# Kernel tuning notes

Hardware: AMD Instinct MI355X
Metric: run time of the kernel (lower is better)

## Reference

```python
import jax, jax.numpy as jnp
import numpy as np
from jax import lax

TAU = 1.0
LAMBDA_CONTRAST = 1.0
GAMMA_ALIGN = 1.0
EPSILON = 0.1
SINKHORN_ITERS = 50
B, V_EN, V_CN, K, H, D = 512, 30000, 20000, 100, 512, 300


def setup_inputs() -> dict:
    key = jax.random.key(0)
    ks = jax.random.split(key, 24)
    s = lambda fan_in: 1.0 / np.sqrt(fan_in)
    inp = {
        'x_bow_en': jax.random.uniform(ks[0], (B, V_EN), jnp.float32),
        'x_bow_cn': jax.random.uniform(ks[1], (B, V_CN), jnp.float32),
        'cluster_ids': jax.random.randint(ks[2], (B,), 0, 9, jnp.int32),
        'eps_en': jax.random.normal(ks[3], (B, K), jnp.float32),
        'eps_cn': jax.random.normal(ks[4], (B, K), jnp.float32),
        # English encoder params
        'W1_en': jax.random.normal(ks[5], (V_EN, H), jnp.float32) * s(V_EN),
        'b1_en': jnp.zeros((H,), jnp.float32),
        'W2_en': jax.random.normal(ks[6], (H, H), jnp.float32) * s(H),
        'b2_en': jnp.zeros((H,), jnp.float32),
        'Wmu_en': jax.random.normal(ks[7], (H, K), jnp.float32) * s(H),
        'bmu_en': jnp.zeros((K,), jnp.float32),
        'Wlv_en': jax.random.normal(ks[8], (H, K), jnp.float32) * s(H),
        'blv_en': jnp.zeros((K,), jnp.float32),
        # Chinese encoder params
        'W1_cn': jax.random.normal(ks[9], (V_CN, H), jnp.float32) * s(V_CN),
        'b1_cn': jnp.zeros((H,), jnp.float32),
        'W2_cn': jax.random.normal(ks[10], (H, H), jnp.float32) * s(H),
        'b2_cn': jnp.zeros((H,), jnp.float32),
        'Wmu_cn': jax.random.normal(ks[11], (H, K), jnp.float32) * s(H),
        'bmu_cn': jnp.zeros((K,), jnp.float32),
        'Wlv_cn': jax.random.normal(ks[12], (H, K), jnp.float32) * s(H),
        'blv_cn': jnp.zeros((K,), jnp.float32),
        # frozen word embeddings + topic embeddings
        'word_emb_en': jax.random.normal(ks[13], (V_EN, D), jnp.float32),
        'word_emb_cn': jax.random.normal(ks[14], (V_CN, D), jnp.float32),
        'topic_emb': jax.random.normal(ks[15], (K, D), jnp.float32),
    }
    return inp


def _encoder(x, eps, W1, b1, W2, b2, Wmu, bmu, Wlv, blv):
    h = jax.nn.softplus(x @ W1 + b1)
    h = jax.nn.softplus(h @ W2 + b2)
    mu = h @ Wmu + bmu
    logvar = h @ Wlv + blv
    z = mu + eps * jnp.exp(0.5 * logvar)  # reparameterization
    theta = jax.nn.softmax(z, axis=-1)
    return theta, mu, logvar


def _compute_beta(word_emb, topic_emb, tau):
    # torch.cdist p=2 -> euclidean distance [V, K]
    sq = (jnp.sum(word_emb ** 2, -1)[:, None] + jnp.sum(topic_emb ** 2, -1)[None, :]
          - 2.0 * word_emb @ topic_emb.T)
    dist = jnp.sqrt(jnp.maximum(sq, 0.0))
    beta = jnp.exp(-dist / tau)
    beta = beta / jnp.sum(beta, axis=0, keepdims=True)  # normalize over vocab
    return beta.T  # [K, V]


def _tm_loss(x_bow, theta, beta, mu, logvar):
    recon = theta @ beta  # [B, V]
    recon_loss = jnp.mean(-jnp.sum(x_bow * jax.nn.log_softmax(recon, axis=-1), axis=-1))
    kl = jnp.mean(0.5 * jnp.sum(jnp.exp(logvar) + mu ** 2 - 1.0 - logvar, axis=-1))
    return recon_loss + kl


def _contrastive_loss(theta_en, theta_cn, cluster_ids, tau):
    b = theta_en.shape[0]
    parity = (jnp.arange(b) % 2 == 0)[:, None]
    thetas = jnp.where(parity, theta_en, theta_cn)  # anchor/other selection
    tn = thetas / jnp.maximum(jnp.linalg.norm(thetas, axis=-1, keepdims=True), 1e-8)
    E = jnp.exp((tn @ tn.T) / tau)  # exp(cos_sim / tau), [B, B]
    offdiag = ~jnp.eye(b, dtype=bool)
    valid = cluster_ids > 0  # falsy cluster -> skipped, matching torch truthiness
    same = cluster_ids[:, None] == cluster_ids[None, :]
    pos_mask = offdiag & same & valid[:, None] & valid[None, :]
    pos_sim = jnp.sum(jnp.where(pos_mask, E, 0.0), axis=1)
    neg_sum = jnp.sum(jnp.where(offdiag, E, 0.0), axis=1)  # all j != i
    has_pos = valid & (jnp.sum(pos_mask, axis=1) > 0)
    per = -jnp.log(pos_sim / (pos_sim + neg_sum + 1e-8))
    loss = jnp.sum(jnp.where(has_pos, per, 0.0))
    count = jnp.sum(has_pos).astype(jnp.float32)
    return loss / (count + 1e-8)


def _sinkhorn(a, b, C, eps):
    Kmat = jnp.exp(-C / eps)
    def step(uv, _):
        u, v = uv
        u = a / (Kmat @ v + 1e-8)
        v = b / (Kmat.T @ u + 1e-8)
        return (u, v), None
    (u, v), _ = lax.scan(step, (jnp.ones_like(a), jnp.ones_like(b)), None, length=SINKHORN_ITERS)
    return u[:, None] * Kmat * v[None, :]


def _alignment_loss(topic_emb, eps):
    tn = topic_emb / jnp.maximum(jnp.linalg.norm(topic_emb, axis=-1, keepdims=True), 1e-8)
    C = 1.0 - tn @ tn.T
    k = topic_emb.shape[0]
    a = jnp.full((k,), 1.0 / k, jnp.float32)
    Q = _sinkhorn(a, a, C, eps)
    return jnp.sum(Q * C)


def reference(x_bow_en, x_bow_cn, cluster_ids, eps_en, eps_cn,
              W1_en, b1_en, W2_en, b2_en, Wmu_en, bmu_en, Wlv_en, blv_en,
              W1_cn, b1_cn, W2_cn, b2_cn, Wmu_cn, bmu_cn, Wlv_cn, blv_cn,
              word_emb_en, word_emb_cn, topic_emb):
    theta_en, mu_en, lv_en = _encoder(x_bow_en, eps_en, W1_en, b1_en, W2_en, b2_en, Wmu_en, bmu_en, Wlv_en, blv_en)
    theta_cn, mu_cn, lv_cn = _encoder(x_bow_cn, eps_cn, W1_cn, b1_cn, W2_cn, b2_cn, Wmu_cn, bmu_cn, Wlv_cn, blv_cn)
    beta_en = _compute_beta(word_emb_en, topic_emb, TAU)
    beta_cn = _compute_beta(word_emb_cn, topic_emb, TAU)
    tm_en = _tm_loss(x_bow_en, theta_en, beta_en, mu_en, lv_en)
    tm_cn = _tm_loss(x_bow_cn, theta_cn, beta_cn, mu_cn, lv_cn)
    contrast = _contrastive_loss(theta_en, theta_cn, cluster_ids, TAU)
    align = _alignment_loss(topic_emb, EPSILON)
    total = tm_en + tm_cn + LAMBDA_CONTRAST * contrast + GAMMA_ALIGN * align
    return total, tm_en, tm_cn, contrast, align, theta_en, theta_cn, beta_en, beta_cn
```

## Files before the change

### kernel.cpp

```cpp
#include <hip/hip_runtime.h>
#include <math.h>

#define BATCH 512
#define VEN 30000
#define VCN 20000
#define KT 100
#define HID 512
#define DIM 300
#define VENP 30080
#define VCNP 20096
#define KDP 320
#define VENK 30080
#define VCNK 20096

typedef float f32x4 __attribute__((ext_vector_type(4)));
typedef short bf16x8 __attribute__((ext_vector_type(8)));
typedef unsigned short u16x8 __attribute__((ext_vector_type(8)));
typedef unsigned int u32;

#define WS_H1_EN   0
#define WS_H2_EN   (WS_H1_EN + 262144)
#define WS_H1_CN   (WS_H2_EN + 262144)
#define WS_H2_CN   (WS_H1_CN + 262144)
#define WS_ROWS_EN (WS_H2_CN + 262144)
#define WS_ROWS_CN (WS_ROWS_EN + 1536)
#define WS_SCAL    (WS_ROWS_CN + 1536)
#define ZERO_FLOATS (WS_SCAL + 64)
#define WS_BIG     ZERO_FLOATS
#define XB_EN      WS_BIG
#define XB_CN      (WS_BIG + 7700480)
#define WEP_EN     WS_BIG
#define WEP_CN     (WS_BIG + 4812800)
#define TEP        (WS_BIG + 4812800 + 3215360)
#define BT_EN      (WS_BIG + 8048640)
#define BT_CN      (BT_EN + 1925120)
#define THP_EN     (BT_CN + 1286144)
#define THP_CN     (THP_EN + 32768)
#define AFTER_BIG  (WS_BIG + 12845056)
#define W1T_EN     AFTER_BIG
#define W1T_CN     (W1T_EN + 7700480)
#define W2T_EN     (W1T_CN + 5144576)
#define W2T_CN     (W2T_EN + 131072)
#define H1B_EN     (W2T_CN + 131072)
#define H1B_CN     (H1B_EN + 131072)
#define WN2_EN     (H1B_CN + 131072)
#define WN2_CN     (WN2_EN + 30080)
#define TN2        (WN2_CN + 20096)
#define WS_TNBUF   (TN2 + 128)
#define WS_TNT     (WS_TNBUF + 51200)
#define WS_CTOP    (WS_TNT + 30000)
#define WS_COLSUM_EN (WS_CTOP + 10000)
#define WS_COLSUM_CN (WS_COLSUM_EN + 128)

#define OUT_THETA_EN 5
#define OUT_THETA_CN (OUT_THETA_EN + 51200)
#define OUT_BETA_EN  (OUT_THETA_CN + 51200)
#define OUT_BETA_CN  (OUT_BETA_EN + 3000000)

__device__ __forceinline__ float waveReduceSum(float v) {
    #pragma unroll
    for (int o = 32; o > 0; o >>= 1) v += __shfl_down(v, o);
    return v;
}

__device__ __forceinline__ unsigned short f2bf(float f) {
    unsigned int u = __float_as_uint(f);
    u = (u + 0x7FFFu + ((u >> 16) & 1u)) >> 16;
    return (unsigned short)u;
}

__device__ __forceinline__ void gl2lds16(const unsigned short* g, unsigned short* l) {
    __builtin_amdgcn_global_load_lds(
        (const __attribute__((address_space(1))) u32*)g,
        (__attribute__((address_space(3))) u32*)l, 16, 0, 0);
}

__global__ __launch_bounds__(256)
void cast_pad_bf16_kernel(const float* __restrict__ src, unsigned short* __restrict__ dst,
                          int cols, int colsPad)
{
    int row = blockIdx.y;
    int col = (blockIdx.x * 256 + threadIdx.x) * 8;
    if (col >= colsPad) return;
    u16x8 o = {0,0,0,0,0,0,0,0};
    if (col < cols) {
        float4 a = *(const float4*)&src[(size_t)row * cols + col];
        float4 b = *(const float4*)&src[(size_t)row * cols + col + 4];
        o = (u16x8){ f2bf(a.x), f2bf(a.y), f2bf(a.z), f2bf(a.w),
                     f2bf(b.x), f2bf(b.y), f2bf(b.z), f2bf(b.w) };
    }
    *(u16x8*)&dst[(size_t)row * colsPad + col] = o;
}

template <int MODE>
__global__ __launch_bounds__(256)
void gemm_async(const unsigned short* __restrict__ A, const unsigned short* __restrict__ B,
                float* __restrict__ C, int N, int ldA, int ldB, int chunkK, int K,
                int Mreal, const float* __restrict__ an2, const float* __restrict__ bn2)
{
    __shared__ __align__(16) unsigned short As[128 * 64];
    __shared__ __align__(16) unsigned short Bs[128 * 64];
    const int tid = threadIdx.x;
    const int m0 = blockIdx.x * 128, n0 = blockIdx.y * 128;
    const int kStart = blockIdx.z * chunkK;
    const int kEnd = min(kStart + chunkK, K);

    const int wave = tid >> 6, lane = tid & 63;
    const int wm = (wave & 1) * 64, wn = (wave >> 1) * 64;
    const int l15 = lane & 15, quad = lane >> 4;

    const int rl = lane >> 3;
    const int cs = (lane & 7) ^ rl;

    f32x4 acc[4][4];
    #pragma unroll
    for (int i = 0; i < 4; ++i)
        #pragma unroll
        for (int j = 0; j < 4; ++j)
            acc[i][j] = (f32x4){0.f, 0.f, 0.f, 0.f};

    for (int k0 = kStart; k0 < kEnd; k0 += 64) {
        #pragma unroll
        for (int j = 0; j < 4; ++j) {
            int seg = wave * 4 + j;
            int r = seg * 8 + rl;
            gl2lds16(A + (size_t)(m0 + r) * ldA + k0 + cs * 8, &As[seg * 512]);
            gl2lds16(B + (size_t)(n0 + r) * ldB + k0 + cs * 8, &Bs[seg * 512]);
        }
        asm volatile("s_waitcnt vmcnt(0)" ::: "memory");
        __syncthreads();

        #pragma unroll
        for (int kh = 0; kh < 2; ++kh) {
            bf16x8 af[4], bfr[4];
            #pragma unroll
            for (int mi = 0; mi < 4; ++mi) {
                int r = wm + mi * 16 + l15;
                af[mi] = *(const bf16x8*)&As[r * 64 + (((kh << 2) | quad) ^ (r & 7)) * 8];
            }
            #pragma unroll
            for (int ni = 0; ni < 4; ++ni) {
                int r = wn + ni * 16 + l15;
                bfr[ni] = *(const bf16x8*)&Bs[r * 64 + (((kh << 2) | quad) ^ (r & 7)) * 8];
            }
            #pragma unroll
            for (int mi = 0; mi < 4; ++mi)
                #pragma unroll
                for (int ni = 0; ni < 4; ++ni)
                    acc[mi][ni] = __builtin_amdgcn_mfma_f32_16x16x32_bf16(af[mi], bfr[ni], acc[mi][ni], 0, 0, 0);
        }
        __syncthreads();
    }

    #pragma unroll
    for (int mi = 0; mi < 4; ++mi)
        #pragma unroll
        for (int ni = 0; ni < 4; ++ni)
            #pragma unroll
            for (int i = 0; i < 4; ++i) {
                int m = m0 + wm + mi * 16 + quad * 4 + i;
                int n = n0 + wn + ni * 16 + l15;
                if (MODE == 0) {
                    atomicAdd(&C[(size_t)m * N + n], acc[mi][ni][i]);
                } else if (MODE == 1) {
                    C[(size_t)m * N + n] = acc[mi][ni][i];
                } else {
                    if (m < Mreal && n < KT) {
                        float sq = an2[m] + bn2[n] - 2.f * acc[mi][ni][i];
                        C[(size_t)n * Mreal + m] = __expf(-sqrtf(fmaxf(sq, 0.f)));
                    }
                }
            }
}

__global__ __launch_bounds__(256)
void recon_mfma_kernel(const unsigned short* __restrict__ A, const unsigned short* __restrict__ B,
                       const float* __restrict__ x, int V, float* __restrict__ rows)
{
    __shared__ __align__(16) unsigned short As[128 * 64];
    __shared__ __align__(16) unsigned short Bs[128 * 64];
    const int tid = threadIdx.x;
    const int m0 = blockIdx.x * 128, n0 = blockIdx.y * 128;
    const int wave = tid >> 6, lane = tid & 63;
    const int wm = (wave & 1) * 64, wn = (wave >> 1) * 64;
    const int l15 = lane & 15, quad = lane >> 4;
    const int rl = lane >> 3;
    const int cs = (lane & 7) ^ rl;

    f32x4 acc[4][4];
    #pragma unroll
    for (int i = 0; i < 4; ++i)
        #pragma unroll
        for (int j = 0; j < 4; ++j)
            acc[i][j] = (f32x4){0.f, 0.f, 0.f, 0.f};

    for (int k0 = 0; k0 < 128; k0 += 64) {
        #pragma unroll
        for (int j = 0; j < 4; ++j) {
            int seg = wave * 4 + j;
            int r = seg * 8 + rl;
            gl2lds16(A + (size_t)(m0 + r) * 128 + k0 + cs * 8, &As[seg * 512]);
            gl2lds16(B + (size_t)(n0 + r) * 128 + k0 + cs * 8, &Bs[seg * 512]);
        }
        asm volatile("s_waitcnt vmcnt(0)" ::: "memory");
        __syncthreads();

        #pragma unroll
        for (int kh = 0; kh < 2; ++kh) {
            bf16x8 af[4], bfr[4];
            #pragma unroll
            for (int mi = 0; mi < 4; ++mi) {
                int r = wm + mi * 16 + l15;
                af[mi] = *(const bf16x8*)&As[r * 64 + (((kh << 2) | quad) ^ (r & 7)) * 8];
            }
            #pragma unroll
            for (int ni = 0; ni < 4; ++ni) {
                int r = wn + ni * 16 + l15;
                bfr[ni] = *(const bf16x8*)&Bs[r * 64 + (((kh << 2) | quad) ^ (r & 7)) * 8];
            }
            #pragma unroll
            for (int mi = 0; mi < 4; ++mi)
                #pragma unroll
                for (int ni = 0; ni < 4; ++ni)
                    acc[mi][ni] = __builtin_amdgcn_mfma_f32_16x16x32_bf16(af[mi], bfr[ni], acc[mi][ni], 0, 0, 0);
        }
        __syncthreads();
    }

    #pragma unroll
    for (int ni = 0; ni < 4; ++ni) {
        int b = n0 + wn + ni * 16 + l15;
        float tse = 0.f, tsxr = 0.f, tsx = 0.f;
        #pragma unroll
        for (int mi = 0; mi < 4; ++mi) {
            int v0 = m0 + wm + mi * 16 + quad * 4;
            if (v0 + 3 < V) {
                float4 xv = *(const float4*)&x[(size_t)b * V + v0];
                float xa[4] = {xv.x, xv.y, xv.z, xv.w};
                #pragma unroll
                for (int i = 0; i < 4; ++i) {
                    float r = acc[mi][ni][i];
                    tse += __expf(r);
                    tsxr += xa[i] * r;
                    tsx  += xa[i];
                }
            } else {
                #pragma unroll
                for (int i = 0; i < 4; ++i) {
                    int v = v0 + i;
                    if (v < V) {
                        float xv1 = x[(size_t)b * V + v];
                        float r = acc[mi][ni][i];
                        tse += __expf(r); tsxr += xv1 * r; tsx += xv1;
                    }
                }
            }
        }
        tse  += __shfl_xor(tse, 16);  tse  += __shfl_xor(tse, 32);
        tsxr += __shfl_xor(tsxr, 16); tsxr += __shfl_xor(tsxr, 32);
        tsx  += __shfl_xor(tsx, 16);  tsx  += __shfl_xor(tsx, 32);
        if (quad == 0) {
            atomicAdd(&rows[b], tse);
            atomicAdd(&rows[512 + b], tsxr);
            atomicAdd(&rows[1024 + b], tsx);
        }
    }
}

__global__ __launch_bounds__(256)
void transpose_cast_kernel(const float* __restrict__ src, unsigned short* __restrict__ dst,
                           int K, int N, int Kp)
{
    __shared__ float tile[32][33];
    int kb = blockIdx.x * 32, nb = blockIdx.y * 32;
    int tx = threadIdx.x & 31, ty4 = threadIdx.x >> 5;
    #pragma unroll
    for (int j = 0; j < 4; ++j) {
        int k = kb + ty4 * 4 + j;
        tile[ty4 * 4 + j][tx] = (k < K) ? src[(size_t)k * N + nb + tx] : 0.f;
    }
    __syncthreads();
    #pragma unroll
    for (int j = 0; j < 4; ++j) {
        int n = nb + ty4 * 4 + j;
        int k = kb + tx;
        if (k < Kp) dst[(size_t)n * Kp + k] = f2bf(tile[tx][ty4 * 4 + j]);
    }
}

__global__ void padcast_sqnorm_kernel(const float* __restrict__ src, unsigned short* __restrict__ dst,
                                      float* __restrict__ n2, int V)
{
    int m = blockIdx.x, tid = threadIdx.x;
    float sq = 0.f;
    #pragma unroll
    for (int j = 0; j < 5; ++j) {
        int k = tid + j * 64;
        float v = (m < V && k < DIM) ? src[(size_t)m * DIM + k] : 0.f;
        dst[(size_t)m * KDP + k] = f2bf(v);
        sq += v * v;
    }
    sq = waveReduceSum(sq);
    if (tid == 0) n2[m] = sq;
}

__global__ __launch_bounds__(256)
void normbeta_bt_kernel(float* __restrict__ beta, const float* __restrict__ cs,
                        unsigned short* __restrict__ bt, int V)
{
    int v = blockIdx.x * 64 + (threadIdx.x & 63);
    int kq = threadIdx.x >> 6;
    unsigned short tmp[32];
    #pragma unroll
    for (int j = 0; j < 32; ++j) {
        int k = kq * 32 + j;
        float val = 0.f;
        if (k < KT && v < V) {
            val = beta[(size_t)k * V + v] * (1.0f / cs[k]);
            beta[(size_t)k * V + v] = val;
        }
        tmp[j] = f2bf(val);
    }
    #pragma unroll
    for (int q = 0; q < 4; ++q)
        *(u16x8*)&bt[(size_t)v * 128 + kq * 32 + q * 8] = *(u16x8*)&tmp[q * 8];
}

__global__ void theta_pad_kernel(const float* __restrict__ theta, unsigned short* __restrict__ thp)
{
    int idx = blockIdx.x * 256 + threadIdx.x;
    int b = idx >> 7, k = idx & 127;
    thp[idx] = f2bf(k < KT ? theta[b * KT + k] : 0.f);
}

__global__ __launch_bounds__(256)
void colsum_kernel(const float* __restrict__ bta, float* __restrict__ cs, int V)
{
    int k = blockIdx.x, tid = threadIdx.x;
    float s = 0.f;
    for (int v = tid; v < V; v += 256) s += bta[(size_t)k * V + v];
    s = waveReduceSum(s);
    __shared__ float cw[4];
    if ((tid & 63) == 0) cw[tid >> 6] = s;
    __syncthreads();
    if (tid == 0) cs[k] = cw[0] + cw[1] + cw[2] + cw[3];
}

__global__ void bias_softplus_bf16_kernel(const float* __restrict__ src, const float* __restrict__ b,
                                          unsigned short* __restrict__ dst, int n)
{
    int i = blockIdx.x * 256 + threadIdx.x;
    if (i < n) {
        float x = src[i] + b[i & (HID - 1)];
        float sp = fmaxf(x, 0.f) + log1pf(__expf(-fabsf(x)));
        dst[i] = f2bf(sp);
    }
}

__global__ void bias_softplus_f32_kernel(float* __restrict__ y, const float* __restrict__ b, int n)
{
    int i = blockIdx.x * 256 + threadIdx.x;
    if (i < n) {
        float x = y[i] + b[i & (HID - 1)];
        y[i] = fmaxf(x, 0.f) + log1pf(__expf(-fabsf(x)));
    }
}

__global__ __launch_bounds__(128)
void encoder_head_kernel(const float* __restrict__ h2, const float* __restrict__ Wmu,
                         const float* __restrict__ bmu, const float* __restrict__ Wlv,
                         const float* __restrict__ blv, const float* __restrict__ eps,
                         float* __restrict__ theta_out, float* __restrict__ kl_accum)
{
    int i = blockIdx.x, tid = threadIdx.x;
    __shared__ float hrow[HID];
    __shared__ float sred[128];
    #pragma unroll
    for (int j = 0; j < 4; ++j) hrow[tid + 128 * j] = h2[i * HID + tid + 128 * j];
    __syncthreads();
    float mu = 0.f, lv = 0.f;
    if (tid < KT) {
        #pragma unroll 8
        for (int h = 0; h < HID; ++h) {
            float hv = hrow[h];
            mu += hv * Wmu[h * KT + tid];
            lv += hv * Wlv[h * KT + tid];
        }
        mu += bmu[tid]; lv += blv[tid];
    }
    float z = (tid < KT) ? (mu + eps[i * KT + tid] * __expf(0.5f * lv)) : -3.0e38f;
    sred[tid] = z; __syncthreads();
    for (int s = 64; s > 0; s >>= 1) { if (tid < s) sred[tid] = fmaxf(sred[tid], sred[tid + s]); __syncthreads(); }
    float zmax = sred[0]; __syncthreads();
    float e = (tid < KT) ? __expf(z - zmax) : 0.f;
    sred[tid] = e; __syncthreads();
    for (int s = 64; s > 0; s >>= 1) { if (tid < s) sred[tid] += sred[tid + s]; __syncthreads(); }
    float esum = sred[0]; __syncthreads();
    if (tid < KT) theta_out[i * KT + tid] = e / esum;
    float kterm = (tid < KT) ? 0.5f * (__expf(lv) + mu * mu - 1.f - lv) : 0.f;
    sred[tid] = kterm; __syncthreads();
    for (int s = 64; s > 0; s >>= 1) { if (tid < s) sred[tid] += sred[tid + s]; __syncthreads(); }
    if (tid == 0) atomicAdd(kl_accum, sred[0]);
}

__global__ __launch_bounds__(256)
void recon_finalize_kernel(const float* __restrict__ rows_en, const float* __restrict__ rows_cn,
                           float* __restrict__ scal)
{
    const float* rows = (blockIdx.x == 0) ? rows_en : rows_cn;
    int tid = threadIdx.x;
    float s = 0.f;
    for (int r = tid; r < 512; r += 256) {
        float se = rows[r], sxr = rows[512 + r], sx = rows[1024 + r];
        s += __logf(se) * sx - sxr;
    }
    s = waveReduceSum(s);
    __shared__ float cw[4];
    if ((tid & 63) == 0) cw[tid >> 6] = s;
    __syncthreads();
    if (tid == 0) scal[5 + blockIdx.x] = cw[0] + cw[1] + cw[2] + cw[3];
}

__global__ __launch_bounds__(128)
void contrast_prep_kernel(const float* __restrict__ theta_en, const float* __restrict__ theta_cn,
                          float* __restrict__ tn)
{
    int i = blockIdx.x, tid = threadIdx.x;
    const float* src = ((i & 1) == 0) ? theta_en : theta_cn;
    float val = (tid < KT) ? src[i * KT + tid] : 0.f;
    __shared__ float sred[128];
    sred[tid] = val * val; __syncthreads();
    for (int s = 64; s > 0; s >>= 1) { if (tid < s) sred[tid] += sred[tid + s]; __syncthreads(); }
    float inv = 1.0f / fmaxf(sqrtf(sred[0]), 1e-8f);
    if (tid < KT) tn[i * KT + tid] = val * inv;
}

__global__ __launch_bounds__(256)
void contrast_main_kernel(const float* __restrict__ tn, const int* __restrict__ cid,
                          float* __restrict__ scal)
{
    int i = blockIdx.x, tid = threadIdx.x;
    __shared__ __align__(16) float ti[KT];
    if (tid < KT) ti[tid] = tn[i * KT + tid];
    __syncthreads();
    int ci = cid[i];
    bool vi = ci > 0;
    float pos = 0.f, neg = 0.f, pcnt = 0.f;
    for (int j = tid; j < 512; j += 256) {
        if (j == i) continue;
        float s = 0.f;
        const float4* tj = reinterpret_cast<const float4*>(&tn[j * KT]);
        #pragma unroll
        for (int q = 0; q < 25; ++q) {
            float4 t4 = tj[q];
            s += ti[4 * q] * t4.x + ti[4 * q + 1] * t4.y + ti[4 * q + 2] * t4.z + ti[4 * q + 3] * t4.w;
        }
        float E = __expf(s);
        neg += E;
        if (vi && cid[j] == ci) { pos += E; pcnt += 1.f; }
    }
    pos = waveReduceSum(pos); neg = waveReduceSum(neg); pcnt = waveReduceSum(pcnt);
    __shared__ float cw[3][4];
    int w = tid >> 6;
    if ((tid & 63) == 0) { cw[0][w] = pos; cw[1][w] = neg; cw[2][w] = pcnt; }
    __syncthreads();
    if (tid == 0) {
        float P = 0.f, N = 0.f, PC = 0.f;
        for (int q = 0; q < 4; ++q) { P += cw[0][q]; N += cw[1][q]; PC += cw[2][q]; }
        if (vi && PC > 0.f) {
            atomicAdd(&scal[2], -__logf(P / (P + N + 1e-8f)));
            atomicAdd(&scal[3], 1.0f);
        }
    }
}

__global__ void norm_rows_kernel(const float* __restrict__ A, float* __restrict__ out, int cols)
{
    int r = blockIdx.x, tid = threadIdx.x;
    float s = 0.f;
    for (int d = tid; d < cols; d += 64) { float a = A[r * cols + d]; s += a * a; }
    s = waveReduceSum(s);
    s = __shfl(s, 0);
    float inv = 1.0f / fmaxf(sqrtf(s), 1e-8f);
    for (int d = tid; d < cols; d += 64) out[r * cols + d] = A[r * cols + d] * inv;
}

__global__ __launch_bounds__(128)
void ctopic_kernel(const float* __restrict__ tnt, float* __restrict__ C)
{
    int i = blockIdx.x, tid = threadIdx.x;
    __shared__ float ti[DIM];
    for (int d = tid; d < DIM; d += 128) ti[d] = tnt[i * DIM + d];
    __syncthreads();
    for (int j = tid; j < KT; j += 128) {
        float s = 0.f;
        for (int d = 0; d < DIM; ++d) s += ti[d] * tnt[j * DIM + d];
        C[i * KT + j] = 1.0f - s;
    }
}

__global__ __launch_bounds__(256, 1)
void sinkhorn_kernel(const float* __restrict__ C, float* __restrict__ scal)
{
    __shared__ __align__(16) float ub[128], vb[128];
    __shared__ float cw[4];
    const int tid = threadIdx.x;
    const bool gA = (tid < 100);
    const bool gB = (tid >= 128 && tid < 228);
    const int rc = gA ? tid : (tid - 128);

    float kk[100];
    if (gA) {
        #pragma unroll
        for (int j = 0; j < 100; ++j) kk[j] = __expf(-10.f * C[rc * 100 + j]);
    } else if (gB) {
        #pragma unroll
        for (int j = 0; j < 100; ++j) kk[j] = __expf(-10.f * C[j * 100 + rc]);
    }
    if (tid < 128) { ub[tid] = 1.f; vb[tid] = 1.f; }
    __syncthreads();

    for (int it = 0; it < 50; ++it) {
        if (gA) {
            float s = 0.f;
            #pragma unroll
            for (int q = 0; q < 25; ++q) {
                float4 v4 = *(const float4*)&vb[q * 4];
                s += kk[q*4]*v4.x + kk[q*4+1]*v4.y + kk[q*4+2]*v4.z + kk[q*4+3]*v4.w;
            }
            ub[rc] = 0.01f / (s + 1e-8f);
        }
        __syncthreads();
        if (gB) {
            float s = 0.f;
            #pragma unroll
            for (int q = 0; q < 25; ++q) {
                float4 u4 = *(const float4*)&ub[q * 4];
                s += kk[q*4]*u4.x + kk[q*4+1]*u4.y + kk[q*4+2]*u4.z + kk[q*4+3]*u4.w;
            }
            vb[rc] = 0.01f / (s + 1e-8f);
        }
        __syncthreads();
    }

    float part = 0.f;
    if (gA) {
        float u = ub[rc];
        #pragma unroll
        for (int j = 0; j < 100; ++j) {
            float k = kk[j];
            part += u * k * vb[j] * (-0.1f * __logf(k));
        }
    }
    part = waveReduceSum(part);
    if ((tid & 63) == 0) cw[tid >> 6] = part;
    __syncthreads();
    if (tid == 0) scal[4] = cw[0] + cw[1] + cw[2] + cw[3];
}

__global__ void final_combine_kernel(const float* __restrict__ scal, float* __restrict__ out)
{
    if (threadIdx.x == 0 && blockIdx.x == 0) {
        const float invB = 1.0f / 512.0f;
        float tm_en = scal[5] * invB + scal[0] * invB;
        float tm_cn = scal[6] * invB + scal[1] * invB;
        float contrast = scal[2] / (scal[3] + 1e-8f);
        float align = scal[4];
        out[0] = tm_en + tm_cn + contrast + align;
        out[1] = tm_en;
        out[2] = tm_cn;
        out[3] = contrast;
        out[4] = align;
    }
}

extern "C" void kernel_launch(void* const* d_in, const int* in_sizes, int n_in,
                              void* d_out_v, int out_size, void* d_ws, size_t ws_size,
                              hipStream_t stream)
{
    const float* x_en   = (const float*)d_in[0];
    const float* x_cn   = (const float*)d_in[1];
    const int*   cid    = (const int*)  d_in[2];
    const float* eps_en = (const float*)d_in[3];
    const float* eps_cn = (const float*)d_in[4];
    const float* W1_en  = (const float*)d_in[5];
    const float* b1_en  = (const float*)d_in[6];
    const float* W2_en  = (const float*)d_in[7];
    const float* b2_en  = (const float*)d_in[8];
    const float* Wmu_en = (const float*)d_in[9];
    const float* bmu_en = (const float*)d_in[10];
    const float* Wlv_en = (const float*)d_in[11];
    const float* blv_en = (const float*)d_in[12];
    const float* W1_cn  = (const float*)d_in[13];
    const float* b1_cn  = (const float*)d_in[14];
    const float* W2_cn  = (const float*)d_in[15];
    const float* b2_cn  = (const float*)d_in[16];
    const float* Wmu_cn = (const float*)d_in[17];
    const float* bmu_cn = (const float*)d_in[18];
    const float* Wlv_cn = (const float*)d_in[19];
    const float* blv_cn = (const float*)d_in[20];
    const float* we_en  = (const float*)d_in[21];
    const float* we_cn  = (const float*)d_in[22];
    const float* te     = (const float*)d_in[23];
    float* out = (float*)d_out_v;
    float* ws  = (float*)d_ws;

    unsigned short* w1t_en = (unsigned short*)(ws + W1T_EN);
    unsigned short* w1t_cn = (unsigned short*)(ws + W1T_CN);
    unsigned short* w2t_en = (unsigned short*)(ws + W2T_EN);
    unsigned short* w2t_cn = (unsigned short*)(ws + W2T_CN);
    unsigned short* h1b_en = (unsigned short*)(ws + H1B_EN);
    unsigned short* h1b_cn = (unsigned short*)(ws + H1B_CN);
    unsigned short* xb_en  = (unsigned short*)(ws + XB_EN);
    unsigned short* xb_cn  = (unsigned short*)(ws + XB_CN);
    unsigned short* wep_en = (unsigned short*)(ws + WEP_EN);
    unsigned short* wep_cn = (unsigned short*)(ws + WEP_CN);
    unsigned short* tep    = (unsigned short*)(ws + TEP);
    unsigned short* bt_en  = (unsigned short*)(ws + BT_EN);
    unsigned short* bt_cn  = (unsigned short*)(ws + BT_CN);
    unsigned short* thp_en = (unsigned short*)(ws + THP_EN);
    unsigned short* thp_cn = (unsigned short*)(ws + THP_CN);

    hipMemsetAsync(d_ws, 0, (size_t)ZERO_FLOATS * sizeof(float), stream);

    cast_pad_bf16_kernel<<<dim3(15, 512), 256, 0, stream>>>(x_en, xb_en, VEN, VENK);
    cast_pad_bf16_kernel<<<dim3(10, 512), 256, 0, stream>>>(x_cn, xb_cn, VCN, VCNK);

    transpose_cast_kernel<<<dim3(940, 16), 256, 0, stream>>>(W1_en, w1t_en, VEN, HID, VENK);
    transpose_cast_kernel<<<dim3(628, 16), 256, 0, stream>>>(W1_cn, w1t_cn, VCN, HID, VCNK);
    transpose_cast_kernel<<<dim3(16, 16), 256, 0, stream>>>(W2_en, w2t_en, HID, HID, HID);
    transpose_cast_kernel<<<dim3(16, 16), 256, 0, stream>>>(W2_cn, w2t_cn, HID, HID, HID);

    gemm_async<0><<<dim3(4, 4, 47), 256, 0, stream>>>(xb_en, w1t_en, ws + WS_H1_EN,
        HID, VENK, VENK, 640, VENK, 0, nullptr, nullptr);
    gemm_async<0><<<dim3(4, 4, 32), 256, 0, stream>>>(xb_cn, w1t_cn, ws + WS_H1_CN,
        HID, VCNK, VCNK, 640, VCNK, 0, nullptr, nullptr);

    bias_softplus_bf16_kernel<<<1024, 256, 0, stream>>>(ws + WS_H1_EN, b1_en, h1b_en, 262144);
    bias_softplus_bf16_kernel<<<1024, 256, 0, stream>>>(ws + WS_H1_CN, b1_cn, h1b_cn, 262144);

    gemm_async<1><<<dim3(4, 4, 1), 256, 0, stream>>>(h1b_en, w2t_en, ws + WS_H2_EN,
        HID, HID, HID, HID, HID, 0, nullptr, nullptr);
    gemm_async<1><<<dim3(4, 4, 1), 256, 0, stream>>>(h1b_cn, w2t_cn, ws + WS_H2_CN,
        HID, HID, HID, HID, HID, 0, nullptr, nullptr);

    bias_softplus_f32_kernel<<<1024, 256, 0, stream>>>(ws + WS_H2_EN, b2_en, 262144);
    bias_softplus_f32_kernel<<<1024, 256, 0, stream>>>(ws + WS_H2_CN, b2_cn, 262144);

    encoder_head_kernel<<<BATCH, 128, 0, stream>>>(ws + WS_H2_EN, Wmu_en, bmu_en, Wlv_en, blv_en,
                                                   eps_en, out + OUT_THETA_EN, ws + WS_SCAL + 0);
    encoder_head_kernel<<<BATCH, 128, 0, stream>>>(ws + WS_H2_CN, Wmu_cn, bmu_cn, Wlv_cn, blv_cn,
                                                   eps_cn, out + OUT_THETA_CN, ws + WS_SCAL + 1);

    padcast_sqnorm_kernel<<<VENP, 64, 0, stream>>>(we_en, wep_en, ws + WN2_EN, VEN);
    padcast_sqnorm_kernel<<<VCNP, 64, 0, stream>>>(we_cn, wep_cn, ws + WN2_CN, VCN);
    padcast_sqnorm_kernel<<<128, 64, 0, stream>>>(te, tep, ws + TN2, KT);

    gemm_async<2><<<dim3(235, 1, 1), 256, 0, stream>>>(wep_en, tep, out + OUT_BETA_EN,
        128, KDP, KDP, KDP, KDP, VEN, ws + WN2_EN, ws + TN2);
    gemm_async<2><<<dim3(157, 1, 1), 256, 0, stream>>>(wep_cn, tep, out + OUT_BETA_CN,
        128, KDP, KDP, KDP, KDP, VCN, ws + WN2_CN, ws + TN2);

    colsum_kernel<<<KT, 256, 0, stream>>>(out + OUT_BETA_EN, ws + WS_COLSUM_EN, VEN);
    colsum_kernel<<<KT, 256, 0, stream>>>(out + OUT_BETA_CN, ws + WS_COLSUM_CN, VCN);

    normbeta_bt_kernel<<<VENP / 64, 256, 0, stream>>>(out + OUT_BETA_EN, ws + WS_COLSUM_EN, bt_en, VEN);
    normbeta_bt_kernel<<<VCNP / 64, 256, 0, stream>>>(out + OUT_BETA_CN, ws + WS_COLSUM_CN, bt_cn, VCN);

    theta_pad_kernel<<<256, 256, 0, stream>>>(out + OUT_THETA_EN, thp_en);
    theta_pad_kernel<<<256, 256, 0, stream>>>(out + OUT_THETA_CN, thp_cn);

    recon_mfma_kernel<<<dim3(VENP / 128, 4), 256, 0, stream>>>(bt_en, thp_en, x_en, VEN, ws + WS_ROWS_EN);
    recon_mfma_kernel<<<dim3(VCNP / 128, 4), 256, 0, stream>>>(bt_cn, thp_cn, x_cn, VCN, ws + WS_ROWS_CN);
    recon_finalize_kernel<<<2, 256, 0, stream>>>(ws + WS_ROWS_EN, ws + WS_ROWS_CN, ws + WS_SCAL);

    contrast_prep_kernel<<<BATCH, 128, 0, stream>>>(out + OUT_THETA_EN, out + OUT_THETA_CN, ws + WS_TNBUF);
    contrast_main_kernel<<<BATCH, 256, 0, stream>>>(ws + WS_TNBUF, cid, ws + WS_SCAL);

    norm_rows_kernel<<<KT, 64, 0, stream>>>(te, ws + WS_TNT, DIM);
    ctopic_kernel<<<KT, 128, 0, stream>>>(ws + WS_TNT, ws + WS_CTOP);
    sinkhorn_kernel<<<1, 256, 0, stream>>>(ws + WS_CTOP, ws + WS_SCAL);

    final_combine_kernel<<<1, 64, 0, stream>>>(ws + WS_SCAL, out);
}
```

Baseline: 887.7 us.

## Merge independent kernels into wide dependency-level launches via block-index dispatch

Replaces about thirty separate kernel launches with roughly nine, each dispatching on block index to the work of one dependency level. Unrelated jobs such as the en/cn encoder stages, beta GEMMs, sinkhorn and the contrastive loss now run concurrently in one grid. Small per-row kernels are repacked so each 256-thread block covers four rows. The aim is to cut launch overhead and fill the GPU during small serial phases. The cost is heterogeneous blocks: every block carries the largest branch's LDS allocation, which can lower occupancy, and a long single-block task such as sinkhorn can set the tail of its launch.

```diff
diff --git a/kernel.cpp b/kernel.cpp
--- a/kernel.cpp
+++ b/kernel.cpp
@@ -75,12 +75,13 @@
         (__attribute__((address_space(3))) u32*)l, 16, 0, 0);
 }
 
-__global__ __launch_bounds__(256)
-void cast_pad_bf16_kernel(const float* __restrict__ src, unsigned short* __restrict__ dst,
-                          int cols, int colsPad)
-{
-    int row = blockIdx.y;
-    int col = (blockIdx.x * 256 + threadIdx.x) * 8;
+
+__device__ __forceinline__ void cast_pad_core(const float* __restrict__ src,
+                                              unsigned short* __restrict__ dst,
+                                              int cols, int colsPad, int nx, int vb)
+{
+    int row = vb / nx, cb = vb - row * nx;
+    int col = (cb * 256 + (int)threadIdx.x) * 8;
     if (col >= colsPad) return;
     u16x8 o = {0,0,0,0,0,0,0,0};
     if (col < cols) {
@@ -92,23 +93,37 @@
     *(u16x8*)&dst[(size_t)row * colsPad + col] = o;
 }
 
+__device__ __forceinline__ void transpose_core(const float* __restrict__ src,
+                                               unsigned short* __restrict__ dst,
+                                               int K, int N, int Kp, int kb, int nb,
+                                               float (*tile)[33])
+{
+    int tx = threadIdx.x & 31, ty4 = threadIdx.x >> 5;
+    #pragma unroll
+    for (int j = 0; j < 4; ++j) {
+        int k = kb + ty4 * 4 + j;
+        tile[ty4 * 4 + j][tx] = (k < K) ? src[(size_t)k * N + nb + tx] : 0.f;
+    }
+    __syncthreads();
+    #pragma unroll
+    for (int j = 0; j < 4; ++j) {
+        int n = nb + ty4 * 4 + j;
+        int k = kb + tx;
+        if (k < Kp) dst[(size_t)n * Kp + k] = f2bf(tile[tx][ty4 * 4 + j]);
+    }
+}
+
 template <int MODE>
-__global__ __launch_bounds__(256)
-void gemm_async(const unsigned short* __restrict__ A, const unsigned short* __restrict__ B,
-                float* __restrict__ C, int N, int ldA, int ldB, int chunkK, int K,
-                int Mreal, const float* __restrict__ an2, const float* __restrict__ bn2)
-{
-    __shared__ __align__(16) unsigned short As[128 * 64];
-    __shared__ __align__(16) unsigned short Bs[128 * 64];
+__device__ __forceinline__ void gemm_core(
+    const unsigned short* __restrict__ A, const unsigned short* __restrict__ B,
+    float* __restrict__ C, int N, int ldA, int ldB, int kStart, int kEnd,
+    int Mreal, const float* __restrict__ an2, const float* __restrict__ bn2,
+    int m0, int n0, unsigned short* As, unsigned short* Bs)
+{
     const int tid = threadIdx.x;
-    const int m0 = blockIdx.x * 128, n0 = blockIdx.y * 128;
-    const int kStart = blockIdx.z * chunkK;
-    const int kEnd = min(kStart + chunkK, K);
-
     const int wave = tid >> 6, lane = tid & 63;
     const int wm = (wave & 1) * 64, wn = (wave >> 1) * 64;
     const int l15 = lane & 15, quad = lane >> 4;
-
     const int rl = lane >> 3;
     const int cs = (lane & 7) ^ rl;
 
@@ -173,14 +188,12 @@
             }
 }
 
-__global__ __launch_bounds__(256)
-void recon_mfma_kernel(const unsigned short* __restrict__ A, const unsigned short* __restrict__ B,
-                       const float* __restrict__ x, int V, float* __restrict__ rows)
-{
-    __shared__ __align__(16) unsigned short As[128 * 64];
-    __shared__ __align__(16) unsigned short Bs[128 * 64];
+__device__ __forceinline__ void recon_core(
+    const unsigned short* __restrict__ A, const unsigned short* __restrict__ B,
+    const float* __restrict__ x, int V, float* __restrict__ rows,
+    int m0, int n0, unsigned short* As, unsigned short* Bs)
+{
     const int tid = threadIdx.x;
-    const int m0 = blockIdx.x * 128, n0 = blockIdx.y * 128;
     const int wave = tid >> 6, lane = tid & 63;
     const int wm = (wave & 1) * 64, wn = (wave >> 1) * 64;
     const int l15 = lane & 15, quad = lane >> 4;
@@ -267,48 +280,112 @@
     }
 }
 
-__global__ __launch_bounds__(256)
-void transpose_cast_kernel(const float* __restrict__ src, unsigned short* __restrict__ dst,
-                           int K, int N, int Kp)
-{
-    __shared__ float tile[32][33];
-    int kb = blockIdx.x * 32, nb = blockIdx.y * 32;
-    int tx = threadIdx.x & 31, ty4 = threadIdx.x >> 5;
-    #pragma unroll
-    for (int j = 0; j < 4; ++j) {
-        int k = kb + ty4 * 4 + j;
-        tile[ty4 * 4 + j][tx] = (k < K) ? src[(size_t)k * N + nb + tx] : 0.f;
-    }
-    __syncthreads();
-    #pragma unroll
-    for (int j = 0; j < 4; ++j) {
-        int n = nb + ty4 * 4 + j;
-        int k = kb + tx;
-        if (k < Kp) dst[(size_t)n * Kp + k] = f2bf(tile[tx][ty4 * 4 + j]);
-    }
-}
-
-__global__ void padcast_sqnorm_kernel(const float* __restrict__ src, unsigned short* __restrict__ dst,
-                                      float* __restrict__ n2, int V)
-{
-    int m = blockIdx.x, tid = threadIdx.x;
+__device__ __forceinline__ void padcast4_core(const float* __restrict__ src,
+                                              unsigned short* __restrict__ dst,
+                                              float* __restrict__ n2, int V, int vb)
+{
+    int w = threadIdx.x >> 6, lane = threadIdx.x & 63;
+    int m = vb * 4 + w;
     float sq = 0.f;
     #pragma unroll
     for (int j = 0; j < 5; ++j) {
-        int k = tid + j * 64;
+        int k = lane + j * 64;
         float v = (m < V && k < DIM) ? src[(size_t)m * DIM + k] : 0.f;
         dst[(size_t)m * KDP + k] = f2bf(v);
         sq += v * v;
     }
     sq = waveReduceSum(sq);
-    if (tid == 0) n2[m] = sq;
-}
-
-__global__ __launch_bounds__(256)
-void normbeta_bt_kernel(float* __restrict__ beta, const float* __restrict__ cs,
-                        unsigned short* __restrict__ bt, int V)
-{
-    int v = blockIdx.x * 64 + (threadIdx.x & 63);
+    if (lane == 0) n2[m] = sq;
+}
+
+__device__ __forceinline__ void norm_rows4_core(const float* __restrict__ A,
+                                                float* __restrict__ out, int vb)
+{
+    int w = threadIdx.x >> 6, lane = threadIdx.x & 63;
+    int r = vb * 4 + w;
+    float s = 0.f;
+    for (int d = lane; d < DIM; d += 64) { float a = A[r * DIM + d]; s += a * a; }
+    s = waveReduceSum(s);
+    s = __shfl(s, 0);
+    float inv = 1.0f / fmaxf(sqrtf(s), 1e-8f);
+    for (int d = lane; d < DIM; d += 64) out[r * DIM + d] = A[r * DIM + d] * inv;
+}
+
+__device__ __forceinline__ void bias_sp_bf16_core(const float* __restrict__ src,
+                                                  const float* __restrict__ b,
+                                                  unsigned short* __restrict__ dst, int vb)
+{
+    int i = vb * 256 + threadIdx.x;
+    float x = src[i] + b[i & (HID - 1)];
+    float sp = fmaxf(x, 0.f) + log1pf(__expf(-fabsf(x)));
+    dst[i] = f2bf(sp);
+}
+
+__device__ __forceinline__ void bias_sp_f32_core(float* __restrict__ y,
+                                                 const float* __restrict__ b, int vb)
+{
+    int i = vb * 256 + threadIdx.x;
+    float x = y[i] + b[i & (HID - 1)];
+    y[i] = fmaxf(x, 0.f) + log1pf(__expf(-fabsf(x)));
+}
+
+__device__ __forceinline__ void encoder_head_core(
+    const float* __restrict__ h2, const float* __restrict__ Wmu, const float* __restrict__ bmu,
+    const float* __restrict__ Wlv, const float* __restrict__ blv, const float* __restrict__ eps,
+    float* __restrict__ theta_out, float* __restrict__ kl_accum, int i,
+    float* hrow, float* red, float* lvb)
+{
+    int tid = threadIdx.x;
+    hrow[tid] = h2[i * HID + tid];
+    hrow[tid + 256] = h2[i * HID + tid + 256];
+    __syncthreads();
+    bool gA = tid < KT;
+    bool gB = (tid >= 128) && (tid < 128 + KT);
+    int rc = gA ? tid : (tid - 128);
+    float acc = 0.f;
+    if (gA || gB) {
+        const float* W = gA ? Wmu : Wlv;
+        #pragma unroll 8
+        for (int h = 0; h < HID; ++h) acc += hrow[h] * W[h * KT + rc];
+        acc += gA ? bmu[rc] : blv[rc];
+    }
+    if (gB) lvb[rc] = acc;
+    __syncthreads();
+    float z = -3.0e38f, kterm = 0.f;
+    if (gA) {
+        float lv = lvb[rc], mu = acc;
+        z = mu + eps[i * KT + rc] * __expf(0.5f * lv);
+        kterm = 0.5f * (__expf(lv) + mu * mu - 1.f - lv);
+    }
+    red[tid] = z; __syncthreads();
+    for (int s = 128; s > 0; s >>= 1) { if (tid < s) red[tid] = fmaxf(red[tid], red[tid + s]); __syncthreads(); }
+    float zmax = red[0]; __syncthreads();
+    float e = gA ? __expf(z - zmax) : 0.f;
+    red[tid] = e; __syncthreads();
+    for (int s = 128; s > 0; s >>= 1) { if (tid < s) red[tid] += red[tid + s]; __syncthreads(); }
+    float esum = red[0]; __syncthreads();
+    if (gA) theta_out[i * KT + rc] = e / esum;
+    red[tid] = gA ? kterm : 0.f; __syncthreads();
+    for (int s = 128; s > 0; s >>= 1) { if (tid < s) red[tid] += red[tid + s]; __syncthreads(); }
+    if (tid == 0) atomicAdd(kl_accum, red[0]);
+}
+
+__device__ __forceinline__ void colsum_core(const float* __restrict__ bta,
+                                            float* __restrict__ cs, int V, int k, float* cw)
+{
+    int tid = threadIdx.x;
+    float s = 0.f;
+    for (int v = tid; v < V; v += 256) s += bta[(size_t)k * V + v];
+    s = waveReduceSum(s);
+    if ((tid & 63) == 0) cw[tid >> 6] = s;
+    __syncthreads();
+    if (tid == 0) cs[k] = cw[0] + cw[1] + cw[2] + cw[3];
+}
+
+__device__ __forceinline__ void normbeta_core(float* __restrict__ beta, const float* __restrict__ cs,
+                                              unsigned short* __restrict__ bt, int V, int vb)
+{
+    int v = vb * 64 + (threadIdx.x & 63);
     int kq = threadIdx.x >> 6;
     unsigned short tmp[32];
     #pragma unroll
@@ -326,121 +403,37 @@
         *(u16x8*)&bt[(size_t)v * 128 + kq * 32 + q * 8] = *(u16x8*)&tmp[q * 8];
 }
 
-__global__ void theta_pad_kernel(const float* __restrict__ theta, unsigned short* __restrict__ thp)
-{
-    int idx = blockIdx.x * 256 + threadIdx.x;
+__device__ __forceinline__ void theta_pad_core(const float* __restrict__ theta,
+                                               unsigned short* __restrict__ thp, int vb)
+{
+    int idx = vb * 256 + threadIdx.x;
     int b = idx >> 7, k = idx & 127;
     thp[idx] = f2bf(k < KT ? theta[b * KT + k] : 0.f);
 }
 
-__global__ __launch_bounds__(256)
-void colsum_kernel(const float* __restrict__ bta, float* __restrict__ cs, int V)
-{
-    int k = blockIdx.x, tid = threadIdx.x;
-    float s = 0.f;
-    for (int v = tid; v < V; v += 256) s += bta[(size_t)k * V + v];
-    s = waveReduceSum(s);
-    __shared__ float cw[4];
-    if ((tid & 63) == 0) cw[tid >> 6] = s;
-    __syncthreads();
-    if (tid == 0) cs[k] = cw[0] + cw[1] + cw[2] + cw[3];
-}
-
-__global__ void bias_softplus_bf16_kernel(const float* __restrict__ src, const float* __restrict__ b,
-                                          unsigned short* __restrict__ dst, int n)
-{
-    int i = blockIdx.x * 256 + threadIdx.x;
-    if (i < n) {
-        float x = src[i] + b[i & (HID - 1)];
-        float sp = fmaxf(x, 0.f) + log1pf(__expf(-fabsf(x)));
-        dst[i] = f2bf(sp);
-    }
-}
-
-__global__ void bias_softplus_f32_kernel(float* __restrict__ y, const float* __restrict__ b, int n)
-{
-    int i = blockIdx.x * 256 + threadIdx.x;
-    if (i < n) {
-        float x = y[i] + b[i & (HID - 1)];
-        y[i] = fmaxf(x, 0.f) + log1pf(__expf(-fabsf(x)));
-    }
-}
-
-__global__ __launch_bounds__(128)
-void encoder_head_kernel(const float* __restrict__ h2, const float* __restrict__ Wmu,
-                         const float* __restrict__ bmu, const float* __restrict__ Wlv,
-                         const float* __restrict__ blv, const float* __restrict__ eps,
-                         float* __restrict__ theta_out, float* __restrict__ kl_accum)
-{
-    int i = blockIdx.x, tid = threadIdx.x;
-    __shared__ float hrow[HID];
-    __shared__ float sred[128];
-    #pragma unroll
-    for (int j = 0; j < 4; ++j) hrow[tid + 128 * j] = h2[i * HID + tid + 128 * j];
-    __syncthreads();
-    float mu = 0.f, lv = 0.f;
-    if (tid < KT) {
-        #pragma unroll 8
-        for (int h = 0; h < HID; ++h) {
-            float hv = hrow[h];
-            mu += hv * Wmu[h * KT + tid];
-            lv += hv * Wlv[h * KT + tid];
-        }
-        mu += bmu[tid]; lv += blv[tid];
-    }
-    float z = (tid < KT) ? (mu + eps[i * KT + tid] * __expf(0.5f * lv)) : -3.0e38f;
-    sred[tid] = z; __syncthreads();
-    for (int s = 64; s > 0; s >>= 1) { if (tid < s) sred[tid] = fmaxf(sred[tid], sred[tid + s]); __syncthreads(); }
-    float zmax = sred[0]; __syncthreads();
-    float e = (tid < KT) ? __expf(z - zmax) : 0.f;
-    sred[tid] = e; __syncthreads();
-    for (int s = 64; s > 0; s >>= 1) { if (tid < s) sred[tid] += sred[tid + s]; __syncthreads(); }
-    float esum = sred[0]; __syncthreads();
-    if (tid < KT) theta_out[i * KT + tid] = e / esum;
-    float kterm = (tid < KT) ? 0.5f * (__expf(lv) + mu * mu - 1.f - lv) : 0.f;
-    sred[tid] = kterm; __syncthreads();
-    for (int s = 64; s > 0; s >>= 1) { if (tid < s) sred[tid] += sred[tid + s]; __syncthreads(); }
-    if (tid == 0) atomicAdd(kl_accum, sred[0]);
-}
-
-__global__ __launch_bounds__(256)
-void recon_finalize_kernel(const float* __restrict__ rows_en, const float* __restrict__ rows_cn,
-                           float* __restrict__ scal)
-{
-    const float* rows = (blockIdx.x == 0) ? rows_en : rows_cn;
+__device__ __forceinline__ void contrast_prep_core(const float* __restrict__ theta_en,
+                                                   const float* __restrict__ theta_cn,
+                                                   float* __restrict__ tn, int vb)
+{
+    int w = threadIdx.x >> 6, lane = threadIdx.x & 63;
+    int i = vb * 4 + w;
+    const float* src = ((i & 1) == 0) ? theta_en : theta_cn;
+    float v0 = (lane < KT) ? src[i * KT + lane] : 0.f;
+    int d1 = lane + 64;
+    float v1 = (d1 < KT) ? src[i * KT + d1] : 0.f;
+    float s = waveReduceSum(v0 * v0 + v1 * v1);
+    s = __shfl(s, 0);
+    float inv = 1.0f / fmaxf(sqrtf(s), 1e-8f);
+    if (lane < KT) tn[i * KT + lane] = v0 * inv;
+    if (d1 < KT) tn[i * KT + d1] = v1 * inv;
+}
+
+__device__ __forceinline__ void contrast_main_core(const float* __restrict__ tn,
+                                                   const int* __restrict__ cid,
+                                                   float* __restrict__ scal, int i,
+                                                   float* ti, float (*cw)[4])
+{
     int tid = threadIdx.x;
-    float s = 0.f;
-    for (int r = tid; r < 512; r += 256) {
-        float se = rows[r], sxr = rows[512 + r], sx = rows[1024 + r];
-        s += __logf(se) * sx - sxr;
-    }
-    s = waveReduceSum(s);
-    __shared__ float cw[4];
-    if ((tid & 63) == 0) cw[tid >> 6] = s;
-    __syncthreads();
-    if (tid == 0) scal[5 + blockIdx.x] = cw[0] + cw[1] + cw[2] + cw[3];
-}
-
-__global__ __launch_bounds__(128)
-void contrast_prep_kernel(const float* __restrict__ theta_en, const float* __restrict__ theta_cn,
-                          float* __restrict__ tn)
-{
-    int i = blockIdx.x, tid = threadIdx.x;
-    const float* src = ((i & 1) == 0) ? theta_en : theta_cn;
-    float val = (tid < KT) ? src[i * KT + tid] : 0.f;
-    __shared__ float sred[128];
-    sred[tid] = val * val; __syncthreads();
-    for (int s = 64; s > 0; s >>= 1) { if (tid < s) sred[tid] += sred[tid + s]; __syncthreads(); }
-    float inv = 1.0f / fmaxf(sqrtf(sred[0]), 1e-8f);
-    if (tid < KT) tn[i * KT + tid] = val * inv;
-}
-
-__global__ __launch_bounds__(256)
-void contrast_main_kernel(const float* __restrict__ tn, const int* __restrict__ cid,
-                          float* __restrict__ scal)
-{
-    int i = blockIdx.x, tid = threadIdx.x;
-    __shared__ __align__(16) float ti[KT];
     if (tid < KT) ti[tid] = tn[i * KT + tid];
     __syncthreads();
     int ci = cid[i];
@@ -460,7 +453,6 @@
         if (vi && cid[j] == ci) { pos += E; pcnt += 1.f; }
     }
     pos = waveReduceSum(pos); neg = waveReduceSum(neg); pcnt = waveReduceSum(pcnt);
-    __shared__ float cw[3][4];
     int w = tid >> 6;
     if ((tid & 63) == 0) { cw[0][w] = pos; cw[1][w] = neg; cw[2][w] = pcnt; }
     __syncthreads();
@@ -474,36 +466,23 @@
     }
 }
 
-__global__ void norm_rows_kernel(const float* __restrict__ A, float* __restrict__ out, int cols)
-{
-    int r = blockIdx.x, tid = threadIdx.x;
-    float s = 0.f;
-    for (int d = tid; d < cols; d += 64) { float a = A[r * cols + d]; s += a * a; }
-    s = waveReduceSum(s);
-    s = __shfl(s, 0);
-    float inv = 1.0f / fmaxf(sqrtf(s), 1e-8f);
-    for (int d = tid; d < cols; d += 64) out[r * cols + d] = A[r * cols + d] * inv;
-}
-
-__global__ __launch_bounds__(128)
-void ctopic_kernel(const float* __restrict__ tnt, float* __restrict__ C)
-{
-    int i = blockIdx.x, tid = threadIdx.x;
-    __shared__ float ti[DIM];
-    for (int d = tid; d < DIM; d += 128) ti[d] = tnt[i * DIM + d];
+__device__ __forceinline__ void ctopic_core(const float* __restrict__ tnt,
+                                            float* __restrict__ C, int i, float* ti)
+{
+    int tid = threadIdx.x;
+    for (int d = tid; d < DIM; d += 256) ti[d] = tnt[i * DIM + d];
     __syncthreads();
-    for (int j = tid; j < KT; j += 128) {
+    for (int j = tid; j < KT; j += 256) {
         float s = 0.f;
         for (int d = 0; d < DIM; ++d) s += ti[d] * tnt[j * DIM + d];
         C[i * KT + j] = 1.0f - s;
     }
 }
 
-__global__ __launch_bounds__(256, 1)
-void sinkhorn_kernel(const float* __restrict__ C, float* __restrict__ scal)
-{
-    __shared__ __align__(16) float ub[128], vb[128];
-    __shared__ float cw[4];
+__device__ __forceinline__ void sinkhorn_core(const float* __restrict__ C,
+                                              float* __restrict__ scal,
+                                              float* ub, float* vbuf, float* cw)
+{
     const int tid = threadIdx.x;
     const bool gA = (tid < 100);
     const bool gB = (tid >= 128 && tid < 228);
@@ -517,7 +496,7 @@
         #pragma unroll
         for (int j = 0; j < 100; ++j) kk[j] = __expf(-10.f * C[j * 100 + rc]);
     }
-    if (tid < 128) { ub[tid] = 1.f; vb[tid] = 1.f; }
+    if (tid < 128) { ub[tid] = 1.f; vbuf[tid] = 1.f; }
     __syncthreads();
 
     for (int it = 0; it < 50; ++it) {
@@ -525,7 +504,7 @@
             float s = 0.f;
             #pragma unroll
             for (int q = 0; q < 25; ++q) {
-                float4 v4 = *(const float4*)&vb[q * 4];
+                float4 v4 = *(const float4*)&vbuf[q * 4];
                 s += kk[q*4]*v4.x + kk[q*4+1]*v4.y + kk[q*4+2]*v4.z + kk[q*4+3]*v4.w;
             }
             ub[rc] = 0.01f / (s + 1e-8f);
@@ -538,7 +517,7 @@
                 float4 u4 = *(const float4*)&ub[q * 4];
                 s += kk[q*4]*u4.x + kk[q*4+1]*u4.y + kk[q*4+2]*u4.z + kk[q*4+3]*u4.w;
             }
-            vb[rc] = 0.01f / (s + 1e-8f);
+            vbuf[rc] = 0.01f / (s + 1e-8f);
         }
         __syncthreads();
     }
@@ -549,7 +528,7 @@
         #pragma unroll
         for (int j = 0; j < 100; ++j) {
             float k = kk[j];
-            part += u * k * vb[j] * (-0.1f * __logf(k));
+            part += u * k * vbuf[j] * (-0.1f * __logf(k));
         }
     }
     part = waveReduceSum(part);
@@ -558,9 +537,187 @@
     if (tid == 0) scal[4] = cw[0] + cw[1] + cw[2] + cw[3];
 }
 
-__global__ void final_combine_kernel(const float* __restrict__ scal, float* __restrict__ out)
-{
-    if (threadIdx.x == 0 && blockIdx.x == 0) {
+
+__global__ __launch_bounds__(256)
+void prep_all_kernel(const float* __restrict__ x_en, const float* __restrict__ x_cn,
+                     const float* __restrict__ W1_en, const float* __restrict__ W1_cn,
+                     const float* __restrict__ W2_en, const float* __restrict__ W2_cn,
+                     unsigned short* xb_en, unsigned short* xb_cn,
+                     unsigned short* w1t_en, unsigned short* w1t_cn,
+                     unsigned short* w2t_en, unsigned short* w2t_cn)
+{
+    __shared__ float tile[32][33];
+    int vb = blockIdx.x;
+    if (vb < 7680) { cast_pad_core(x_en, xb_en, VEN, VENK, 15, vb); }
+    else if (vb < 12800) { cast_pad_core(x_cn, xb_cn, VCN, VCNK, 10, vb - 7680); }
+    else if (vb < 27840) { int v = vb - 12800; transpose_core(W1_en, w1t_en, VEN, HID, VENK, (v % 940) * 32, (v / 940) * 32, tile); }
+    else if (vb < 37888) { int v = vb - 27840; transpose_core(W1_cn, w1t_cn, VCN, HID, VCNK, (v % 628) * 32, (v / 628) * 32, tile); }
+    else if (vb < 38144) { int v = vb - 37888; transpose_core(W2_en, w2t_en, HID, HID, HID, (v & 15) * 32, (v >> 4) * 32, tile); }
+    else { int v = vb - 38144; transpose_core(W2_cn, w2t_cn, HID, HID, HID, (v & 15) * 32, (v >> 4) * 32, tile); }
+}
+
+__global__ __launch_bounds__(256)
+void gemm1_both_kernel(const unsigned short* __restrict__ xb_en, const unsigned short* __restrict__ w1t_en,
+                       float* __restrict__ h1_en,
+                       const unsigned short* __restrict__ xb_cn, const unsigned short* __restrict__ w1t_cn,
+                       float* __restrict__ h1_cn)
+{
+    __shared__ __align__(16) unsigned short As[128 * 64];
+    __shared__ __align__(16) unsigned short Bs[128 * 64];
+    int vb = blockIdx.x;
+    if (vb < 752) {
+        int z = vb >> 4, xy = vb & 15;
+        gemm_core<0>(xb_en, w1t_en, h1_en, HID, VENK, VENK, z * 640, min(z * 640 + 640, VENK),
+                     0, nullptr, nullptr, (xy & 3) * 128, (xy >> 2) * 128, As, Bs);
+    } else {
+        int v = vb - 752;
+        int z = v >> 4, xy = v & 15;
+        gemm_core<0>(xb_cn, w1t_cn, h1_cn, HID, VCNK, VCNK, z * 640, min(z * 640 + 640, VCNK),
+                     0, nullptr, nullptr, (xy & 3) * 128, (xy >> 2) * 128, As, Bs);
+    }
+}
+
+__global__ __launch_bounds__(256)
+void bias1_both_kernel(const float* __restrict__ h1_en, const float* __restrict__ b1_en,
+                       unsigned short* __restrict__ h1b_en,
+                       const float* __restrict__ h1_cn, const float* __restrict__ b1_cn,
+                       unsigned short* __restrict__ h1b_cn)
+{
+    int vb = blockIdx.x;
+    if (vb < 1024) bias_sp_bf16_core(h1_en, b1_en, h1b_en, vb);
+    else bias_sp_bf16_core(h1_cn, b1_cn, h1b_cn, vb - 1024);
+}
+
+__global__ __launch_bounds__(256)
+void d5_kernel(const unsigned short* __restrict__ h1b_en, const unsigned short* __restrict__ w2t_en,
+               float* __restrict__ h2_en,
+               const unsigned short* __restrict__ h1b_cn, const unsigned short* __restrict__ w2t_cn,
+               float* __restrict__ h2_cn,
+               const float* __restrict__ we_en, unsigned short* __restrict__ wep_en, float* __restrict__ wn2_en,
+               const float* __restrict__ we_cn, unsigned short* __restrict__ wep_cn, float* __restrict__ wn2_cn,
+               const float* __restrict__ te, unsigned short* __restrict__ tep, float* __restrict__ tn2,
+               float* __restrict__ tnt)
+{
+    __shared__ __align__(16) unsigned short As[128 * 64];
+    __shared__ __align__(16) unsigned short Bs[128 * 64];
+    int vb = blockIdx.x;
+    if (vb < 16) {
+        gemm_core<1>(h1b_en, w2t_en, h2_en, HID, HID, HID, 0, HID,
+                     0, nullptr, nullptr, (vb & 3) * 128, (vb >> 2) * 128, As, Bs);
+    } else if (vb < 32) {
+        int v = vb - 16;
+        gemm_core<1>(h1b_cn, w2t_cn, h2_cn, HID, HID, HID, 0, HID,
+                     0, nullptr, nullptr, (v & 3) * 128, (v >> 2) * 128, As, Bs);
+    }
+    else if (vb < 7552) padcast4_core(we_en, wep_en, wn2_en, VEN, vb - 32);
+    else if (vb < 12576) padcast4_core(we_cn, wep_cn, wn2_cn, VCN, vb - 7552);
+    else if (vb < 12608) padcast4_core(te, tep, tn2, KT, vb - 12576);
+    else norm_rows4_core(te, tnt, vb - 12608);
+}
+
+__global__ __launch_bounds__(256)
+void d6_kernel(float* __restrict__ h2_en, const float* __restrict__ b2_en,
+               float* __restrict__ h2_cn, const float* __restrict__ b2_cn,
+               const float* __restrict__ tnt, float* __restrict__ ctop,
+               const unsigned short* __restrict__ wep_en, const unsigned short* __restrict__ tep,
+               float* __restrict__ beta_en, const float* __restrict__ wn2_en, const float* __restrict__ tn2,
+               const unsigned short* __restrict__ wep_cn, float* __restrict__ beta_cn,
+               const float* __restrict__ wn2_cn)
+{
+    __shared__ __align__(16) unsigned short As[128 * 64];
+    __shared__ __align__(16) unsigned short Bs[128 * 64];
+    __shared__ float ti[DIM];
+    int vb = blockIdx.x;
+    if (vb < 1024) bias_sp_f32_core(h2_en, b2_en, vb);
+    else if (vb < 2048) bias_sp_f32_core(h2_cn, b2_cn, vb - 1024);
+    else if (vb < 2148) ctopic_core(tnt, ctop, vb - 2048, ti);
+    else if (vb < 2383) {
+        gemm_core<2>(wep_en, tep, beta_en, 128, KDP, KDP, 0, KDP,
+                     VEN, wn2_en, tn2, (vb - 2148) * 128, 0, As, Bs);
+    } else {
+        gemm_core<2>(wep_cn, tep, beta_cn, 128, KDP, KDP, 0, KDP,
+                     VCN, wn2_cn, tn2, (vb - 2383) * 128, 0, As, Bs);
+    }
+}
+
+__global__ __launch_bounds__(256)
+void d7_kernel(const float* __restrict__ h2_en, const float* __restrict__ Wmu_en,
+               const float* __restrict__ bmu_en, const float* __restrict__ Wlv_en,
+               const float* __restrict__ blv_en, const float* __restrict__ eps_en,
+               float* __restrict__ theta_en,
+               const float* __restrict__ h2_cn, const float* __restrict__ Wmu_cn,
+               const float* __restrict__ bmu_cn, const float* __restrict__ Wlv_cn,
+               const float* __restrict__ blv_cn, const float* __restrict__ eps_cn,
+               float* __restrict__ theta_cn,
+               const float* __restrict__ beta_en, float* __restrict__ cs_en,
+               const float* __restrict__ beta_cn, float* __restrict__ cs_cn,
+               const float* __restrict__ ctop, float* __restrict__ scal)
+{
+    __shared__ float hrow[HID];
+    __shared__ float red[256];
+    __shared__ float lvb[128];
+    __shared__ float cw[4];
+    int vb = blockIdx.x;
+    if (vb < 512) encoder_head_core(h2_en, Wmu_en, bmu_en, Wlv_en, blv_en, eps_en, theta_en, &scal[0], vb, hrow, red, lvb);
+    else if (vb < 1024) encoder_head_core(h2_cn, Wmu_cn, bmu_cn, Wlv_cn, blv_cn, eps_cn, theta_cn, &scal[1], vb - 512, hrow, red, lvb);
+    else if (vb < 1124) colsum_core(beta_en, cs_en, VEN, vb - 1024, cw);
+    else if (vb < 1224) colsum_core(beta_cn, cs_cn, VCN, vb - 1124, cw);
+    else sinkhorn_core(ctop, scal, red, lvb, cw);
+}
+
+__global__ __launch_bounds__(256)
+void d8_kernel(float* __restrict__ beta_en, const float* __restrict__ cs_en, unsigned short* __restrict__ bt_en,
+               float* __restrict__ beta_cn, const float* __restrict__ cs_cn, unsigned short* __restrict__ bt_cn,
+               const float* __restrict__ theta_en, unsigned short* __restrict__ thp_en,
+               const float* __restrict__ theta_cn, unsigned short* __restrict__ thp_cn,
+               float* __restrict__ tn)
+{
+    int vb = blockIdx.x;
+    if (vb < 470) normbeta_core(beta_en, cs_en, bt_en, VEN, vb);
+    else if (vb < 784) normbeta_core(beta_cn, cs_cn, bt_cn, VCN, vb - 470);
+    else if (vb < 1040) theta_pad_core(theta_en, thp_en, vb - 784);
+    else if (vb < 1296) theta_pad_core(theta_cn, thp_cn, vb - 1040);
+    else contrast_prep_core(theta_en, theta_cn, tn, vb - 1296);
+}
+
+__global__ __launch_bounds__(256)
+void d9_kernel(const unsigned short* __restrict__ bt_en, const unsigned short* __restrict__ thp_en,
+               const float* __restrict__ x_en, float* __restrict__ rows_en,
+               const unsigned short* __restrict__ bt_cn, const unsigned short* __restrict__ thp_cn,
+               const float* __restrict__ x_cn, float* __restrict__ rows_cn,
+               const float* __restrict__ tn, const int* __restrict__ cid, float* __restrict__ scal)
+{
+    __shared__ __align__(16) unsigned short As[128 * 64];
+    __shared__ __align__(16) unsigned short Bs[128 * 64];
+    __shared__ float ti[KT];
+    __shared__ float cw[3][4];
+    int vb = blockIdx.x;
+    if (vb < 940) recon_core(bt_en, thp_en, x_en, VEN, rows_en, (vb % 235) * 128, (vb / 235) * 128, As, Bs);
+    else if (vb < 1568) { int v = vb - 940; recon_core(bt_cn, thp_cn, x_cn, VCN, rows_cn, (v % 157) * 128, (v / 157) * 128, As, Bs); }
+    else contrast_main_core(tn, cid, scal, vb - 1568, ti, cw);
+}
+
+__global__ __launch_bounds__(256)
+void finalize_kernel(const float* __restrict__ rows_en, const float* __restrict__ rows_cn,
+                     float* __restrict__ scal, float* __restrict__ out)
+{
+    __shared__ float cw[4];
+    int tid = threadIdx.x;
+    #pragma unroll
+    for (int side = 0; side < 2; ++side) {
+        const float* rows = side ? rows_cn : rows_en;
+        float s = 0.f;
+        for (int r = tid; r < 512; r += 256) {
+            float se = rows[r], sxr = rows[512 + r], sx = rows[1024 + r];
+            s += __logf(se) * sx - sxr;
+        }
+        s = waveReduceSum(s);
+        if ((tid & 63) == 0) cw[tid >> 6] = s;
+        __syncthreads();
+        if (tid == 0) scal[5 + side] = cw[0] + cw[1] + cw[2] + cw[3];
+        __syncthreads();
+    }
+    if (tid == 0) {
         const float invB = 1.0f / 512.0f;
         float tm_en = scal[5] * invB + scal[0] * invB;
         float tm_cn = scal[6] * invB + scal[1] * invB;
@@ -623,63 +780,43 @@
 
     hipMemsetAsync(d_ws, 0, (size_t)ZERO_FLOATS * sizeof(float), stream);
 
-    cast_pad_bf16_kernel<<<dim3(15, 512), 256, 0, stream>>>(x_en, xb_en, VEN, VENK);
-    cast_pad_bf16_kernel<<<dim3(10, 512), 256, 0, stream>>>(x_cn, xb_cn, VCN, VCNK);
-
-    transpose_cast_kernel<<<dim3(940, 16), 256, 0, stream>>>(W1_en, w1t_en, VEN, HID, VENK);
-    transpose_cast_kernel<<<dim3(628, 16), 256, 0, stream>>>(W1_cn, w1t_cn, VCN, HID, VCNK);
-    transpose_cast_kernel<<<dim3(16, 16), 256, 0, stream>>>(W2_en, w2t_en, HID, HID, HID);
-    transpose_cast_kernel<<<dim3(16, 16), 256, 0, stream>>>(W2_cn, w2t_cn, HID, HID, HID);
-
-    gemm_async<0><<<dim3(4, 4, 47), 256, 0, stream>>>(xb_en, w1t_en, ws + WS_H1_EN,
-        HID, VENK, VENK, 640, VENK, 0, nullptr, nullptr);
-    gemm_async<0><<<dim3(4, 4, 32), 256, 0, stream>>>(xb_cn, w1t_cn, ws + WS_H1_CN,
-        HID, VCNK, VCNK, 640, VCNK, 0, nullptr, nullptr);
-
-    bias_softplus_bf16_kernel<<<1024, 256, 0, stream>>>(ws + WS_H1_EN, b1_en, h1b_en, 262144);
-    bias_softplus_bf16_kernel<<<1024, 256, 0, stream>>>(ws + WS_H1_CN, b1_cn, h1b_cn, 262144);
-
-    gemm_async<1><<<dim3(4, 4, 1), 256, 0, stream>>>(h1b_en, w2t_en, ws + WS_H2_EN,
-        HID, HID, HID, HID, HID, 0, nullptr, nullptr);
-    gemm_async<1><<<dim3(4, 4, 1), 256, 0, stream>>>(h1b_cn, w2t_cn, ws + WS_H2_CN,
-        HID, HID, HID, HID, HID, 0, nullptr, nullptr);
-
-    bias_softplus_f32_kernel<<<1024, 256, 0, stream>>>(ws + WS_H2_EN, b2_en, 262144);
-    bias_softplus_f32_kernel<<<1024, 256, 0, stream>>>(ws + WS_H2_CN, b2_cn, 262144);
-
-    encoder_head_kernel<<<BATCH, 128, 0, stream>>>(ws + WS_H2_EN, Wmu_en, bmu_en, Wlv_en, blv_en,
-                                                   eps_en, out + OUT_THETA_EN, ws + WS_SCAL + 0);
-    encoder_head_kernel<<<BATCH, 128, 0, stream>>>(ws + WS_H2_CN, Wmu_cn, bmu_cn, Wlv_cn, blv_cn,
-                                                   eps_cn, out + OUT_THETA_CN, ws + WS_SCAL + 1);
-
-    padcast_sqnorm_kernel<<<VENP, 64, 0, stream>>>(we_en, wep_en, ws + WN2_EN, VEN);
-    padcast_sqnorm_kernel<<<VCNP, 64, 0, stream>>>(we_cn, wep_cn, ws + WN2_CN, VCN);
-    padcast_sqnorm_kernel<<<128, 64, 0, stream>>>(te, tep, ws + TN2, KT);
-
-    gemm_async<2><<<dim3(235, 1, 1), 256, 0, stream>>>(wep_en, tep, out + OUT_BETA_EN,
-        128, KDP, KDP, KDP, KDP, VEN, ws + WN2_EN, ws + TN2);
-    gemm_async<2><<<dim3(157, 1, 1), 256, 0, stream>>>(wep_cn, tep, out + OUT_BETA_CN,
-        128, KDP, KDP, KDP, KDP, VCN, ws + WN2_CN, ws + TN2);
-
-    colsum_kernel<<<KT, 256, 0, stream>>>(out + OUT_BETA_EN, ws + WS_COLSUM_EN, VEN);
-    colsum_kernel<<<KT, 256, 0, stream>>>(out + OUT_BETA_CN, ws + WS_COLSUM_CN, VCN);
-
-    normbeta_bt_kernel<<<VENP / 64, 256, 0, stream>>>(out + OUT_BETA_EN, ws + WS_COLSUM_EN, bt_en, VEN);
-    normbeta_bt_kernel<<<VCNP / 64, 256, 0, stream>>>(out + OUT_BETA_CN, ws + WS_COLSUM_CN, bt_cn, VCN);
-
-    theta_pad_kernel<<<256, 256, 0, stream>>>(out + OUT_THETA_EN, thp_en);
-    theta_pad_kernel<<<256, 256, 0, stream>>>(out + OUT_THETA_CN, thp_cn);
-
-    recon_mfma_kernel<<<dim3(VENP / 128, 4), 256, 0, stream>>>(bt_en, thp_en, x_en, VEN, ws + WS_ROWS_EN);
-    recon_mfma_kernel<<<dim3(VCNP / 128, 4), 256, 0, stream>>>(bt_cn, thp_cn, x_cn, VCN, ws + WS_ROWS_CN);
-    recon_finalize_kernel<<<2, 256, 0, stream>>>(ws + WS_ROWS_EN, ws + WS_ROWS_CN, ws + WS_SCAL);
-
-    contrast_prep_kernel<<<BATCH, 128, 0, stream>>>(out + OUT_THETA_EN, out + OUT_THETA_CN, ws + WS_TNBUF);
-    contrast_main_kernel<<<BATCH, 256, 0, stream>>>(ws + WS_TNBUF, cid, ws + WS_SCAL);
-
-    norm_rows_kernel<<<KT, 64, 0, stream>>>(te, ws + WS_TNT, DIM);
-    ctopic_kernel<<<KT, 128, 0, stream>>>(ws + WS_TNT, ws + WS_CTOP);
-    sinkhorn_kernel<<<1, 256, 0, stream>>>(ws + WS_CTOP, ws + WS_SCAL);
-
-    final_combine_kernel<<<1, 64, 0, stream>>>(ws + WS_SCAL, out);
-}
+    prep_all_kernel<<<38400, 256, 0, stream>>>(x_en, x_cn, W1_en, W1_cn, W2_en, W2_cn,
+                                               xb_en, xb_cn, w1t_en, w1t_cn, w2t_en, w2t_cn);
+
+    gemm1_both_kernel<<<1264, 256, 0, stream>>>(xb_en, w1t_en, ws + WS_H1_EN,
+                                                xb_cn, w1t_cn, ws + WS_H1_CN);
+
+    bias1_both_kernel<<<2048, 256, 0, stream>>>(ws + WS_H1_EN, b1_en, h1b_en,
+                                                ws + WS_H1_CN, b1_cn, h1b_cn);
+
+    d5_kernel<<<12633, 256, 0, stream>>>(h1b_en, w2t_en, ws + WS_H2_EN,
+                                         h1b_cn, w2t_cn, ws + WS_H2_CN,
+                                         we_en, wep_en, ws + WN2_EN,
+                                         we_cn, wep_cn, ws + WN2_CN,
+                                         te, tep, ws + TN2, ws + WS_TNT);
+
+    d6_kernel<<<2540, 256, 0, stream>>>(ws + WS_H2_EN, b2_en, ws + WS_H2_CN, b2_cn,
+                                        ws + WS_TNT, ws + WS_CTOP,
+                                        wep_en, tep, out + OUT_BETA_EN, ws + WN2_EN, ws + TN2,
+                                        wep_cn, out + OUT_BETA_CN, ws + WN2_CN);
+
+    d7_kernel<<<1225, 256, 0, stream>>>(ws + WS_H2_EN, Wmu_en, bmu_en, Wlv_en, blv_en, eps_en,
+                                        out + OUT_THETA_EN,
+                                        ws + WS_H2_CN, Wmu_cn, bmu_cn, Wlv_cn, blv_cn, eps_cn,
+                                        out + OUT_THETA_CN,
+                                        out + OUT_BETA_EN, ws + WS_COLSUM_EN,
+                                        out + OUT_BETA_CN, ws + WS_COLSUM_CN,
+                                        ws + WS_CTOP, ws + WS_SCAL);
+
+    d8_kernel<<<1424, 256, 0, stream>>>(out + OUT_BETA_EN, ws + WS_COLSUM_EN, bt_en,
+                                        out + OUT_BETA_CN, ws + WS_COLSUM_CN, bt_cn,
+                                        out + OUT_THETA_EN, thp_en,
+                                        out + OUT_THETA_CN, thp_cn,
+                                        ws + WS_TNBUF);
+
+    d9_kernel<<<2080, 256, 0, stream>>>(bt_en, thp_en, x_en, ws + WS_ROWS_EN,
+                                        bt_cn, thp_cn, x_cn, ws + WS_ROWS_CN,
+                                        ws + WS_TNBUF, cid, ws + WS_SCAL);
+
+    finalize_kernel<<<1, 256, 0, stream>>>(ws + WS_ROWS_EN, ws + WS_ROWS_CN, ws + WS_SCAL, out);
+}
```

Measured after the change: 748.8 us. 15.6% less time.
